# Kernel optimization log

Hardware: AMD Instinct MI355X
Metric: run time of the kernel (lower is better)

Reference implementation:

```python
import jax, jax.numpy as jnp
import numpy as np

B, S, D, H = 4, 2048, 1024, 16
HD = D // H

def setup_inputs() -> dict:
    key = jax.random.key(0)
    ks = jax.random.split(key, 11)
    s = 1.0 / np.sqrt(D)
    return {
        "q": jax.random.normal(ks[0], (B, S, D), jnp.float32),
        "k": jax.random.normal(ks[1], (B, S, D), jnp.float32),
        "v": jax.random.normal(ks[2], (B, S, D), jnp.float32),
        "Wq": jax.random.normal(ks[3], (D, D), jnp.float32) * s,
        "bq": jax.random.normal(ks[4], (D,), jnp.float32) * 0.01,
        "Wk": jax.random.normal(ks[5], (D, D), jnp.float32) * s,
        "bk": jax.random.normal(ks[6], (D,), jnp.float32) * 0.01,
        "Wv": jax.random.normal(ks[7], (D, D), jnp.float32) * s,
        "bv": jax.random.normal(ks[8], (D,), jnp.float32) * 0.01,
        "Wo": jax.random.normal(ks[9], (D, D), jnp.float32) * s,
        "bo": jax.random.normal(ks[10], (D,), jnp.float32) * 0.01,
    }

def reference(q, k, v, Wq, bq, Wk, bk, Wv, bv, Wo, bo):
    # linear projections + ReLU activation (as in the torch module)
    qh = jax.nn.relu(q @ Wq.T + bq)
    kh = jax.nn.relu(k @ Wk.T + bk)
    vh = jax.nn.relu(v @ Wv.T + bv)
    # split heads: [B,S,D] -> [B,H,S,HD]
    def split(x):
        return x.reshape(B, S, H, HD).transpose(0, 2, 1, 3)
    qh, kh, vh = split(qh), split(kh), split(vh)
    scale = 1.0 / np.sqrt(HD).astype(np.float32)
    scores = jnp.einsum("bhqd,bhkd->bhqk", qh, kh) * scale
    attn = jax.nn.softmax(scores, axis=-1)
    y = jnp.einsum("bhqk,bhkd->bhqd", attn, vh)
    # merge heads: [B,H,S,HD] -> [B,S,D]
    y = y.transpose(0, 2, 1, 3).reshape(B, S, D)
    return jax.nn.relu(y @ Wo.T + bo)
```

## Files before the change

kernel.cpp:

```cpp
#include <hip/hip_runtime.h>
#include <hip/hip_bf16.h>
#include <cstdint>
#include <cstddef>

#define Bc 4
#define Sc 2048
#define Dc 1024
#define Hc 16

typedef __bf16 bf16;
typedef bf16  bf16x4 __attribute__((ext_vector_type(4)));
typedef bf16  bf16x8 __attribute__((ext_vector_type(8)));
typedef float f32x4  __attribute__((ext_vector_type(4)));

__device__ __forceinline__ void load_lds16(const bf16* g, bf16* l) {
    __builtin_amdgcn_global_load_lds((const __attribute__((address_space(1))) void*)g,
                                     (__attribute__((address_space(3))) void*)l,
                                     16, 0, 0);
}

__device__ __forceinline__ void cvt16(const float* __restrict__ g,
                                      bf16x8& lo, bf16x8& hi) {
    const f32x4 a0 = *(const f32x4*)(g);
    const f32x4 a1 = *(const f32x4*)(g + 4);
    const f32x4 a2 = *(const f32x4*)(g + 8);
    const f32x4 a3 = *(const f32x4*)(g + 12);
#pragma unroll
    for (int j = 0; j < 4; j++) {
        lo[j]     = (bf16)a0[j];
        lo[j + 4] = (bf16)a1[j];
        hi[j]     = (bf16)a2[j];
        hi[j + 4] = (bf16)a3[j];
    }
}

__device__ __forceinline__ void store_relu(float* p, float v) { *p = fmaxf(v, 0.0f); }
__device__ __forceinline__ void store_relu(bf16*  p, float v) { *p = (bf16)fmaxf(v, 0.0f); }

__global__ __launch_bounds__(256)
void cvt_f32_bf16(const float* __restrict__ src, bf16* __restrict__ dst, int n16) {
    const int idx = blockIdx.x * 256 + threadIdx.x;
    if (idx >= n16) return;
    bf16x8 lo, hi;
    cvt16(src + (size_t)idx * 16, lo, hi);
    *(bf16x8*)(dst + (size_t)idx * 16)     = lo;
    *(bf16x8*)(dst + (size_t)idx * 16 + 8) = hi;
}

#define BM 128
#define BN 128
#define BK 64

template <typename TC, bool TR>
__global__ __launch_bounds__(256)
void gemm_bb(const bf16* __restrict__ A, const bf16* __restrict__ W,
             const float* __restrict__ bias, TC* __restrict__ C,
             int M, int N, int K) {
    constexpr int POOL = TR ? 36864 : 32768;
    __shared__ __align__(16) char pool[POOL];
    bf16* lA = (bf16*)pool;
    bf16* lB = (bf16*)(pool + 16384);

    const int t    = threadIdx.x;
    const int lane = t & 63;
    const int wave = t >> 6;
    const int l15  = lane & 15;
    const int quad = lane >> 4;

    const int m0 = blockIdx.x * BM;
    const int n0 = blockIdx.y * BN;
    const int wm = (wave >> 1) * 64;
    const int wn = (wave & 1) * 64;

    f32x4 acc[4][4] = {};

    const int srow = t >> 3;
    const int cg   = (((t & 7) ^ (srow & 7)) << 3);
    const bf16* gA = A + (size_t)(m0 + srow) * K + cg;
    const bf16* gW = W + (size_t)(n0 + srow) * K + cg;
    bf16* lA0 = lA + t * 8;
    bf16* lB0 = lB + t * 8;

    for (int k0 = 0; k0 < K; k0 += BK) {
        __syncthreads();
#pragma unroll
        for (int c = 0; c < 4; c++) {
            load_lds16(gA + (size_t)(32 * c) * K, lA0 + c * 2048);
            load_lds16(gW + (size_t)(32 * c) * K, lB0 + c * 2048);
        }
        gA += BK; gW += BK;
        __syncthreads();

#pragma unroll
        for (int ks = 0; ks < 2; ks++) {
            bf16x8 af[4], bfr[4];
#pragma unroll
            for (int mt = 0; mt < 4; mt++) {
                const int row = wm + mt * 16 + l15;
                const int colp = ((((ks << 2) | quad) ^ (l15 & 7)) << 3);
                af[mt] = *(const bf16x8*)(lA + row * BK + colp);
            }
#pragma unroll
            for (int nt = 0; nt < 4; nt++) {
                const int row = wn + nt * 16 + l15;
                const int colp = ((((ks << 2) | quad) ^ (l15 & 7)) << 3);
                bfr[nt] = *(const bf16x8*)(lB + row * BK + colp);
            }
#pragma unroll
            for (int mt = 0; mt < 4; mt++)
#pragma unroll
                for (int nt = 0; nt < 4; nt++)
                    acc[mt][nt] = __builtin_amdgcn_mfma_f32_16x16x32_bf16(
                        af[mt], bfr[nt], acc[mt][nt], 0, 0, 0);
        }
    }

    if constexpr (!TR) {
#pragma unroll
        for (int nt = 0; nt < 4; nt++) {
            const int col = n0 + wn + nt * 16 + l15;
            const float bv = bias[col];
#pragma unroll
            for (int mt = 0; mt < 4; mt++) {
                const int rowb = m0 + wm + mt * 16 + quad * 4;
#pragma unroll
                for (int i = 0; i < 4; i++)
                    store_relu(&C[(size_t)(rowb + i) * N + col], acc[mt][nt][i] + bv);
            }
        }
    } else {
        __syncthreads();
        bf16* trp = (bf16*)pool;
#pragma unroll
        for (int nt = 0; nt < 4; nt++) {
            const int col = n0 + wn + nt * 16 + l15;
            const float bv = bias[col];
#pragma unroll
            for (int mt = 0; mt < 4; mt++)
#pragma unroll
                for (int i = 0; i < 4; i++)
                    trp[((wave * 64) + nt * 16 + l15) * 72 + mt * 16 + quad * 4 + i] =
                        (bf16)fmaxf(acc[mt][nt][i] + bv, 0.0f);
        }
        __syncthreads();
        const int r2 = lane >> 3;
        const int c8 = (lane & 7) * 8;
#pragma unroll
        for (int rr = 0; rr < 8; rr++) {
            const int rt = rr * 8 + r2;
            const bf16x8 vv = *(const bf16x8*)&trp[((wave * 64) + rt) * 72 + c8];
            const int cg2 = n0 + wn + rt;
            const int h   = cg2 >> 6, hd = cg2 & 63;
            const int mg  = m0 + wm + c8;
            const int b   = mg >> 11, s = mg & (Sc - 1);
            bf16* dst = (bf16*)C + ((size_t)(b * Hc + h) * 64 + hd) * Sc + s;
            *(bf16x8*)dst = vv;
        }
    }
}

#define QI 4

__global__ __launch_bounds__(256)
void attn_flash(const bf16* __restrict__ Qh, const bf16* __restrict__ Kh,
                const bf16* __restrict__ Vt_g, bf16* __restrict__ Y) {
    __shared__ __align__(16) bf16 Kl[64][72];
    __shared__ __align__(16) bf16 Vl[64][72];
    __shared__ __align__(16) bf16 Pl[4][2][16][72];

    const int t    = threadIdx.x;
    const int lane = t & 63;
    const int wave = t >> 6;
    const int l15  = lane & 15;
    const int quad = lane >> 4;

    const int qt = blockIdx.x;
    const int bh = blockIdx.y;
    const int b  = bh >> 4;
    const int h  = bh & 15;
    const int q0 = qt * 256;
    const size_t rowbase = (size_t)b * Sc;
    const size_t vhead   = (size_t)(b * Hc + h) * 64;

    const float qscale = 0.125f * 1.44269504f;
    bf16x8 qf[QI][2];
#pragma unroll
    for (int qi = 0; qi < QI; qi++) {
        const bf16* qp = Qh + (rowbase + q0 + wave * 64 + qi * 16 + l15) * (size_t)Dc + h * 64;
#pragma unroll
        for (int ks = 0; ks < 2; ks++) {
            const bf16x8 raw = *(const bf16x8*)(qp + ks * 32 + quad * 8);
#pragma unroll
            for (int j = 0; j < 8; j++) qf[qi][ks][j] = (bf16)((float)raw[j] * qscale);
        }
    }

    bf16x8 ones;
#pragma unroll
    for (int j = 0; j < 8; j++) ones[j] = (bf16)1.0f;

    f32x4 yacc[QI][4] = {};
    f32x4 sacc[QI]    = {};

    const int sr = t >> 2;
    const int sc = (t & 3) * 16;

    for (int kt = 0; kt < Sc / 64; kt++) {
        const int kb = kt * 64;
        const bf16* kp = Kh + (rowbase + kb + sr) * (size_t)Dc + h * 64 + sc;
        const bf16* vp = Vt_g + (vhead + sr) * (size_t)Sc + kb + sc;
        const bf16x8 k0 = *(const bf16x8*)kp;
        const bf16x8 k1 = *(const bf16x8*)(kp + 8);
        const bf16x8 v0 = *(const bf16x8*)vp;
        const bf16x8 v1 = *(const bf16x8*)(vp + 8);
        __syncthreads();
        *(bf16x8*)&Kl[sr][sc]     = k0;
        *(bf16x8*)&Kl[sr][sc + 8] = k1;
        *(bf16x8*)&Vl[sr][sc]     = v0;
        *(bf16x8*)&Vl[sr][sc + 8] = v1;
        __syncthreads();

        bf16x8 kf[4][2], vf[4][2];
#pragma unroll
        for (int mt = 0; mt < 4; mt++) {
            kf[mt][0] = *(const bf16x8*)&Kl[mt * 16 + l15][quad * 8];
            kf[mt][1] = *(const bf16x8*)&Kl[mt * 16 + l15][32 + quad * 8];
        }
#pragma unroll
        for (int nt = 0; nt < 4; nt++) {
            vf[nt][0] = *(const bf16x8*)&Vl[nt * 16 + l15][quad * 8];
            vf[nt][1] = *(const bf16x8*)&Vl[nt * 16 + l15][32 + quad * 8];
        }

#pragma unroll
        for (int qi = 0; qi < QI; qi++) {
            const int slot = qi & 1;
            f32x4 s[4];
            __builtin_amdgcn_s_setprio(1);
#pragma unroll
            for (int mt = 0; mt < 4; mt++) {
                s[mt] = (f32x4){0.f, 0.f, 0.f, 0.f};
                s[mt] = __builtin_amdgcn_mfma_f32_16x16x32_bf16(
                    kf[mt][0], qf[qi][0], s[mt], 0, 0, 0);
                s[mt] = __builtin_amdgcn_mfma_f32_16x16x32_bf16(
                    kf[mt][1], qf[qi][1], s[mt], 0, 0, 0);
            }
            __builtin_amdgcn_s_setprio(0);

#pragma unroll
            for (int mt = 0; mt < 4; mt++) {
                bf16x4 pk;
#pragma unroll
                for (int i = 0; i < 4; i++)
                    pk[i] = (bf16)exp2f(s[mt][i]);
                *(bf16x4*)&Pl[wave][slot][l15][mt * 16 + quad * 4] = pk;
            }

            const bf16x8 pf0 = *(const bf16x8*)&Pl[wave][slot][l15][quad * 8];
            const bf16x8 pf1 = *(const bf16x8*)&Pl[wave][slot][l15][32 + quad * 8];

            __builtin_amdgcn_s_setprio(1);
            sacc[qi] = __builtin_amdgcn_mfma_f32_16x16x32_bf16(ones, pf0, sacc[qi], 0, 0, 0);
            sacc[qi] = __builtin_amdgcn_mfma_f32_16x16x32_bf16(ones, pf1, sacc[qi], 0, 0, 0);
#pragma unroll
            for (int nt = 0; nt < 4; nt++) {
                yacc[qi][nt] = __builtin_amdgcn_mfma_f32_16x16x32_bf16(
                    vf[nt][0], pf0, yacc[qi][nt], 0, 0, 0);
                yacc[qi][nt] = __builtin_amdgcn_mfma_f32_16x16x32_bf16(
                    vf[nt][1], pf1, yacc[qi][nt], 0, 0, 0);
            }
            __builtin_amdgcn_s_setprio(0);
        }
    }

#pragma unroll
    for (int qi = 0; qi < QI; qi++) {
        const float inv = 1.0f / sacc[qi][0];
        bf16* yp = Y + (rowbase + q0 + wave * 64 + qi * 16 + l15) * (size_t)Dc + h * 64;
#pragma unroll
        for (int nt = 0; nt < 4; nt++)
#pragma unroll
            for (int i = 0; i < 4; i++)
                yp[nt * 16 + quad * 4 + i] = (bf16)(yacc[qi][nt][i] * inv);
    }
}

extern "C" void kernel_launch(void* const* d_in, const int* in_sizes, int n_in,
                              void* d_out, int out_size, void* d_ws, size_t ws_size,
                              hipStream_t stream) {
    const float* q  = (const float*)d_in[0];
    const float* k  = (const float*)d_in[1];
    const float* v  = (const float*)d_in[2];
    const float* Wq = (const float*)d_in[3];
    const float* bq = (const float*)d_in[4];
    const float* Wk = (const float*)d_in[5];
    const float* bk = (const float*)d_in[6];
    const float* Wv = (const float*)d_in[7];
    const float* bv = (const float*)d_in[8];
    const float* Wo = (const float*)d_in[9];
    const float* bo = (const float*)d_in[10];
    float* out = (float*)d_out;

    const int M = Bc * Sc;
    const int N = Dc;
    const int K = Dc;
    const size_t E  = (size_t)Bc * Sc * Dc;
    const size_t EW = (size_t)Dc * Dc;

    bf16* Qh   = (bf16*)d_out;
    bf16* Kh   = Qh + E;
    bf16* tmpA = (bf16*)d_ws;
    bf16* VtG  = tmpA + E;
    bf16* Wqb  = VtG + E;
    bf16* Wkb  = Wqb + EW;
    bf16* Wvb  = Wkb + EW;
    bf16* Wob  = Wvb + EW;

    const int n16  = (int)(E / 16);
    const int n16w = (int)(EW / 16);
    dim3 gc(n16 / 256);
    dim3 gw(n16w / 256);
    dim3 gg(M / BM, N / BN);
    dim3 ga(Sc / 256, Bc * Hc);

    cvt_f32_bf16<<<gw, 256, 0, stream>>>(Wq, Wqb, n16w);
    cvt_f32_bf16<<<gw, 256, 0, stream>>>(Wk, Wkb, n16w);
    cvt_f32_bf16<<<gw, 256, 0, stream>>>(Wv, Wvb, n16w);
    cvt_f32_bf16<<<gw, 256, 0, stream>>>(Wo, Wob, n16w);

    cvt_f32_bf16<<<gc, 256, 0, stream>>>(q, tmpA, n16);
    gemm_bb<bf16, false><<<gg, 256, 0, stream>>>(tmpA, Wqb, bq, Qh, M, N, K);

    cvt_f32_bf16<<<gc, 256, 0, stream>>>(k, tmpA, n16);
    gemm_bb<bf16, false><<<gg, 256, 0, stream>>>(tmpA, Wkb, bk, Kh, M, N, K);

    cvt_f32_bf16<<<gc, 256, 0, stream>>>(v, tmpA, n16);
    gemm_bb<bf16, true><<<gg, 256, 0, stream>>>(tmpA, Wvb, bv, VtG, M, N, K);

    attn_flash<<<ga, 256, 0, stream>>>(Qh, Kh, VtG, tmpA);

    gemm_bb<float, false><<<gg, 256, 0, stream>>>(tmpA, Wob, bo, out, M, N, K);
}
```

Baseline: 390.8 us.

## Prefetch next K/V tile into registers and split attention into QK and PV phases

Global loads for the next K/V tile are now issued right after the LDS store barrier, so their latency overlaps with the current tile's compute. The inner loop is split into two phases: all QK MFMAs plus exp writes P for every query block into a larger per-wave LDS buffer, then all PV MFMAs run back-to-back. exp2f is replaced by the hardware exp2 intrinsic. The cost is more LDS (a full 64x72 P buffer per wave) and higher register pressure from prefetch registers and pf[QI][2], which may reduce occupancy.

```diff
diff --git a/kernel.cpp b/kernel.cpp
--- a/kernel.cpp
+++ b/kernel.cpp
@@ -166,7 +166,7 @@
                 const bf16* __restrict__ Vt_g, bf16* __restrict__ Y) {
     __shared__ __align__(16) bf16 Kl[64][72];
     __shared__ __align__(16) bf16 Vl[64][72];
-    __shared__ __align__(16) bf16 Pl[4][2][16][72];
+    __shared__ __align__(16) bf16 Pl[4][64][72];
 
     const int t    = threadIdx.x;
     const int lane = t & 63;
@@ -204,15 +204,16 @@
 
     const int sr = t >> 2;
     const int sc = (t & 3) * 16;
-
-    for (int kt = 0; kt < Sc / 64; kt++) {
-        const int kb = kt * 64;
-        const bf16* kp = Kh + (rowbase + kb + sr) * (size_t)Dc + h * 64 + sc;
-        const bf16* vp = Vt_g + (vhead + sr) * (size_t)Sc + kb + sc;
-        const bf16x8 k0 = *(const bf16x8*)kp;
-        const bf16x8 k1 = *(const bf16x8*)(kp + 8);
-        const bf16x8 v0 = *(const bf16x8*)vp;
-        const bf16x8 v1 = *(const bf16x8*)(vp + 8);
+    constexpr int NT = Sc / 64;
+
+    const bf16* kp = Kh + (rowbase + sr) * (size_t)Dc + h * 64 + sc;
+    const bf16* vp = Vt_g + (vhead + sr) * (size_t)Sc + sc;
+    bf16x8 k0 = *(const bf16x8*)kp;
+    bf16x8 k1 = *(const bf16x8*)(kp + 8);
+    bf16x8 v0 = *(const bf16x8*)vp;
+    bf16x8 v1 = *(const bf16x8*)(vp + 8);
+
+    for (int kt = 0; kt < NT; kt++) {
         __syncthreads();
         *(bf16x8*)&Kl[sr][sc]     = k0;
         *(bf16x8*)&Kl[sr][sc + 8] = k1;
@@ -220,21 +221,24 @@
         *(bf16x8*)&Vl[sr][sc + 8] = v1;
         __syncthreads();
 
-        bf16x8 kf[4][2], vf[4][2];
+        if (kt + 1 < NT) {
+            kp += (size_t)64 * Dc;
+            vp += 64;
+            k0 = *(const bf16x8*)kp;
+            k1 = *(const bf16x8*)(kp + 8);
+            v0 = *(const bf16x8*)vp;
+            v1 = *(const bf16x8*)(vp + 8);
+        }
+
+        bf16x8 kf[4][2];
 #pragma unroll
         for (int mt = 0; mt < 4; mt++) {
             kf[mt][0] = *(const bf16x8*)&Kl[mt * 16 + l15][quad * 8];
             kf[mt][1] = *(const bf16x8*)&Kl[mt * 16 + l15][32 + quad * 8];
         }
-#pragma unroll
-        for (int nt = 0; nt < 4; nt++) {
-            vf[nt][0] = *(const bf16x8*)&Vl[nt * 16 + l15][quad * 8];
-            vf[nt][1] = *(const bf16x8*)&Vl[nt * 16 + l15][32 + quad * 8];
-        }
 
 #pragma unroll
         for (int qi = 0; qi < QI; qi++) {
-            const int slot = qi & 1;
             f32x4 s[4];
             __builtin_amdgcn_s_setprio(1);
 #pragma unroll
@@ -246,31 +250,43 @@
                     kf[mt][1], qf[qi][1], s[mt], 0, 0, 0);
             }
             __builtin_amdgcn_s_setprio(0);
-
 #pragma unroll
             for (int mt = 0; mt < 4; mt++) {
                 bf16x4 pk;
 #pragma unroll
                 for (int i = 0; i < 4; i++)
-                    pk[i] = (bf16)exp2f(s[mt][i]);
-                *(bf16x4*)&Pl[wave][slot][l15][mt * 16 + quad * 4] = pk;
-            }
-
-            const bf16x8 pf0 = *(const bf16x8*)&Pl[wave][slot][l15][quad * 8];
-            const bf16x8 pf1 = *(const bf16x8*)&Pl[wave][slot][l15][32 + quad * 8];
-
-            __builtin_amdgcn_s_setprio(1);
-            sacc[qi] = __builtin_amdgcn_mfma_f32_16x16x32_bf16(ones, pf0, sacc[qi], 0, 0, 0);
-            sacc[qi] = __builtin_amdgcn_mfma_f32_16x16x32_bf16(ones, pf1, sacc[qi], 0, 0, 0);
+                    pk[i] = (bf16)__builtin_amdgcn_exp2f(s[mt][i]);
+                *(bf16x4*)&Pl[wave][qi * 16 + l15][mt * 16 + quad * 4] = pk;
+            }
+        }
+
+        bf16x8 vf[4][2];
+#pragma unroll
+        for (int nt = 0; nt < 4; nt++) {
+            vf[nt][0] = *(const bf16x8*)&Vl[nt * 16 + l15][quad * 8];
+            vf[nt][1] = *(const bf16x8*)&Vl[nt * 16 + l15][32 + quad * 8];
+        }
+
+        bf16x8 pf[QI][2];
+#pragma unroll
+        for (int qi = 0; qi < QI; qi++) {
+            pf[qi][0] = *(const bf16x8*)&Pl[wave][qi * 16 + l15][quad * 8];
+            pf[qi][1] = *(const bf16x8*)&Pl[wave][qi * 16 + l15][32 + quad * 8];
+        }
+        __builtin_amdgcn_s_setprio(1);
+#pragma unroll
+        for (int qi = 0; qi < QI; qi++) {
+            sacc[qi] = __builtin_amdgcn_mfma_f32_16x16x32_bf16(ones, pf[qi][0], sacc[qi], 0, 0, 0);
+            sacc[qi] = __builtin_amdgcn_mfma_f32_16x16x32_bf16(ones, pf[qi][1], sacc[qi], 0, 0, 0);
 #pragma unroll
             for (int nt = 0; nt < 4; nt++) {
                 yacc[qi][nt] = __builtin_amdgcn_mfma_f32_16x16x32_bf16(
-                    vf[nt][0], pf0, yacc[qi][nt], 0, 0, 0);
+                    vf[nt][0], pf[qi][0], yacc[qi][nt], 0, 0, 0);
                 yacc[qi][nt] = __builtin_amdgcn_mfma_f32_16x16x32_bf16(
-                    vf[nt][1], pf1, yacc[qi][nt], 0, 0, 0);
-            }
-            __builtin_amdgcn_s_setprio(0);
-        }
+                    vf[nt][1], pf[qi][1], yacc[qi][nt], 0, 0, 0);
+            }
+        }
+        __builtin_amdgcn_s_setprio(0);
     }
 
 #pragma unroll
```

Measured after the change: 379.7 us. -2.9%, faster.
